# Optimization experiments

Measured on AMD Instinct MI355X. Metric: run time of the kernel, lower is better.

Reference implementation:

```python
import jax, jax.numpy as jnp
import numpy as np

D_MODEL, D_STATE, D_INNER, DT_RANK, D_CONV, K = 768, 16, 1536, 48, 3, 2
B_SZ, L_SEQ = 2, 2048

def setup_inputs() -> dict:
    key = jax.random.key(0)
    ks = jax.random.split(key, 10)
    s = lambda k, shp, sc=0.02: jax.random.normal(k, shp, dtype=jnp.float32) * sc
    return {
        "x": jax.random.normal(ks[0], (B_SZ, L_SEQ, D_MODEL), dtype=jnp.float32),
        "in_proj_w": s(ks[1], (2 * D_INNER, D_MODEL)),
        "conv_w": s(ks[2], (D_INNER, 1, D_CONV), 0.3),
        "conv_b": s(ks[3], (D_INNER,), 0.1),
        "x_proj_w": s(ks[4], (K, DT_RANK + 2 * D_STATE, D_INNER)),
        "dt_proj_w": s(ks[5], (K, D_INNER, DT_RANK), 0.1),
        "dt_proj_b": s(ks[6], (K, D_INNER), 0.1),
        "A_logs": s(ks[7], (K * D_INNER, D_STATE), 0.5),
        "Ds": jnp.ones((K * D_INNER,), dtype=jnp.float32),
        "out_proj_w": s(ks[8], (D_MODEL, D_INNER)),
    }

def _selective_scan(u, delta, A, Bp, Cp, Dk):
    # u, delta: [B, L, D]; A: [D, N]; Bp, Cp: [B, L, N]; Dk: [D]
    def step(h, inp):
        d_t, u_t, b_t, c_t = inp  # [B,D], [B,D], [B,N], [B,N]
        dA = jnp.exp(d_t[..., None] * A)  # [B,D,N]
        h = h * dA + (d_t * u_t)[..., None] * b_t[:, None, :]
        y_t = jnp.einsum('bdn,bn->bd', h, c_t)
        return h, y_t
    h0 = jnp.zeros((u.shape[0], u.shape[2], A.shape[1]), dtype=u.dtype)
    xs = (jnp.swapaxes(delta, 0, 1), jnp.swapaxes(u, 0, 1),
          jnp.swapaxes(Bp, 0, 1), jnp.swapaxes(Cp, 0, 1))
    _, ys = jax.lax.scan(step, h0, xs)  # ys: [L, B, D]
    return jnp.swapaxes(ys, 0, 1) + u * Dk  # [B, L, D]

def _direction(u_k, xw_k, dtw_k, dtb_k, Alog_k, D_k):
    x_dbl = jnp.einsum('bld,rd->blr', u_k, xw_k)
    dt_in, Bp, Cp = jnp.split(x_dbl, [DT_RANK, DT_RANK + D_STATE], axis=-1)
    delta = jax.nn.softplus(jnp.einsum('blr,dr->bld', dt_in, dtw_k) + dtb_k)
    A = -jnp.exp(Alog_k)
    return _selective_scan(u_k, delta, A, Bp, Cp, D_k)

def reference(x, in_proj_w, conv_w, conv_b, x_proj_w, dt_proj_w, dt_proj_b, A_logs, Ds, out_proj_w):
    xz = x @ in_proj_w.T                       # [B, L, 2*Din]
    x_conv, z = jnp.split(xz, 2, axis=-1)
    xc = jnp.swapaxes(x_conv, 1, 2)            # [B, Din, L]
    pad = (D_CONV - 1) // 2
    xc = jax.lax.conv_general_dilated(
        xc, conv_w, window_strides=(1,), padding=[(pad, pad)],
        feature_group_count=D_INNER, dimension_numbers=('NCH', 'OIH', 'NCH'))
    xc = xc + conv_b[None, :, None]
    u = jnp.swapaxes(jax.nn.silu(xc), 1, 2)    # [B, L, Din]

    u_dirs = jnp.stack([u, jnp.flip(u, axis=1)])          # [K, B, L, Din]
    A_logs_k = A_logs.reshape(K, D_INNER, D_STATE)
    Ds_k = Ds.reshape(K, D_INNER)
    y_dirs = jax.vmap(_direction)(u_dirs, x_proj_w, dt_proj_w, dt_proj_b, A_logs_k, Ds_k)
    y_scanned = y_dirs[0] + jnp.flip(y_dirs[1], axis=1)
    y_gated = y_scanned * z
    return y_gated @ out_proj_w.T
```

## Files before the change

kernel.cpp:

```cpp
#include <hip/hip_runtime.h>
#include <math.h>

#define D_MODEL 768
#define D_STATE 16
#define D_INNER 1536
#define DT_RANK 48
#define B_SZ    2
#define L_SEQ   2048
#define CH      64
#define NCH     (L_SEQ / CH)
#define NDG     24
#define MTOT    (B_SZ * L_SEQ)
#define SUB     16
#define LOG2E   1.4426950408889634f
#define LN2     0.6931471805599453f

typedef __bf16 bf16x8 __attribute__((ext_vector_type(8)));
typedef float f32x4 __attribute__((ext_vector_type(4)));
typedef ushort ushort8_t __attribute__((ext_vector_type(8)));

__device__ __forceinline__ float ex2(float x) {
  return __builtin_amdgcn_exp2f(x);
}

__device__ __forceinline__ ushort f2bf(float f) {
  unsigned int u = __float_as_uint(f);
  unsigned int r = (u + 0x7fff + ((u >> 16) & 1)) >> 16;
  return (ushort)r;
}
__device__ __forceinline__ float bf2f(ushort u) {
  return __uint_as_float(((unsigned int)u) << 16);
}

__device__ __forceinline__ void gload_lds16(const ushort* g, ushort* l) {
  __builtin_amdgcn_global_load_lds(
      (__attribute__((address_space(1))) void*)(void*)(g),
      (__attribute__((address_space(3))) void*)(void*)(l), 16, 0, 0);
}

__device__ __forceinline__ float softplus_fast(float x) {
  return (x > 20.f) ? x : LN2 * __log2f(1.f + ex2(x * LOG2E));
}

template <int BM, int BN, int ACT, int OBF, int DTOUT>
__device__ __forceinline__ void gemm_body(
    const ushort* __restrict__ A, int lda, const ushort* __restrict__ B,
    int ldb, const float* __restrict__ bias, void* __restrict__ Cp, int ldc,
    int Nreal, int K, int bxi, int byi, ushort* __restrict__ dtin,
    ushort* __restrict__ bcp) {
  __shared__ ushort As[2][BM][32];
  __shared__ ushort Bs[2][BN][32];
  constexpr int WM = BM / 2, WN = BN / 2;
  constexpr int FM = WM / 16, FN = WN / 16;
  const int tid = threadIdx.x;
  const int lane = tid & 63;
  const int w = tid >> 6;
  const int wr = w >> 1, wc = w & 1;
  const int bm = byi * BM, bn = bxi * BN;
  const int lrow = lane >> 2;
  const int lchunk = lane & 3;
  const int fr = lane & 15;
  const int k8 = (lane >> 4) * 8;

  f32x4 acc[FM][FN] = {};

  auto stage = [&](int buf, int k0) {
    if constexpr (BM >= 64) {
#pragma unroll
      for (int g = 0; g < BM / 64; ++g) {
        const int rb = w * (BM / 4) + g * 16;
        gload_lds16(A + (size_t)(bm + rb + lrow) * lda + k0 + lchunk * 8,
                    &As[buf][rb][0]);
      }
    } else {
      if (w < 2)
        gload_lds16(A + (size_t)(bm + w * 16 + lrow) * lda + k0 + lchunk * 8,
                    &As[buf][w * 16][0]);
    }
#pragma unroll
    for (int g = 0; g < BN / 64; ++g) {
      const int rb = w * (BN / 4) + g * 16;
      gload_lds16(B + (size_t)(bn + rb + lrow) * ldb + k0 + lchunk * 8,
                  &Bs[buf][rb][0]);
    }
  };

  stage(0, 0);
  __syncthreads();
  int cur = 0;
  for (int k0 = 0; k0 < K; k0 += 32) {
    if (k0 + 32 < K) stage(cur ^ 1, k0 + 32);
    bf16x8 af[FM], bfr[FN];
#pragma unroll
    for (int m = 0; m < FM; ++m)
      af[m] =
          *reinterpret_cast<const bf16x8*>(&As[cur][wr * WM + m * 16 + fr][k8]);
#pragma unroll
    for (int n = 0; n < FN; ++n)
      bfr[n] =
          *reinterpret_cast<const bf16x8*>(&Bs[cur][wc * WN + n * 16 + fr][k8]);
#pragma unroll
    for (int m = 0; m < FM; ++m)
#pragma unroll
      for (int n = 0; n < FN; ++n)
        acc[m][n] = __builtin_amdgcn_mfma_f32_16x16x32_bf16(af[m], bfr[n],
                                                            acc[m][n], 0, 0, 0);
    __syncthreads();
    cur ^= 1;
  }

  const int row4 = (lane >> 4) * 4;
#pragma unroll
  for (int m = 0; m < FM; ++m) {
#pragma unroll
    for (int n = 0; n < FN; ++n) {
      const int gn = bn + wc * WN + n * 16 + fr;
      const int gm0 = bm + wr * WM + m * 16 + row4;
#pragma unroll
      for (int j = 0; j < 4; ++j) {
        const float v = acc[m][n][j];
        const int gm = gm0 + j;
        if (DTOUT) {
          if (gn < 64)
            dtin[(size_t)gm * 64 + gn] = (gn < 48) ? f2bf(v) : (ushort)0;
          else if (gn >= 80 && gn < 144)
            dtin[(size_t)MTOT * 64 + (size_t)gm * 64 + (gn - 80)] =
                (gn < 128) ? f2bf(v) : (ushort)0;
          if (gn >= 48 && gn < 80)
            bcp[(size_t)gm * 32 + (gn - 48)] = f2bf(v);
          else if (gn >= 128 && gn < 160)
            bcp[(size_t)MTOT * 32 + (size_t)gm * 32 + (gn - 128)] = f2bf(v);
        }
        if (gn < Nreal) {
          float vv = v + (bias ? bias[gn] : 0.f);
          if (ACT == 1) vv = softplus_fast(vv);
          if (OBF)
            ((ushort*)Cp)[(size_t)gm * ldc + gn] = f2bf(vv);
          else
            ((float*)Cp)[(size_t)gm * ldc + gn] = vv;
        }
      }
    }
  }
}

template <int BM, int BN, int ACT, int OBF, int DTOUT>
__global__ __launch_bounds__(256) void gemm_k(
    const ushort* __restrict__ A, int lda, const ushort* __restrict__ B,
    int ldb, const float* __restrict__ bias, void* __restrict__ Cp, int ldc,
    int Nreal, int K, ushort* __restrict__ dtin, ushort* __restrict__ bcp) {
  gemm_body<BM, BN, ACT, OBF, DTOUT>(A, lda, B, ldb, bias, Cp, ldc, Nreal, K,
                                     blockIdx.x, blockIdx.y, dtin, bcp);
}

__global__ __launch_bounds__(256) void gemm_dt_k(
    const ushort* __restrict__ dtin, const ushort* __restrict__ w_dt,
    const float* __restrict__ dtb, ushort* __restrict__ delta) {
  const int k = blockIdx.z;
  gemm_body<64, 128, 1, 1, 0>(
      dtin + (size_t)k * MTOT * 64, 64, w_dt + (size_t)k * D_INNER * 64, 64,
      dtb + k * D_INNER, delta + (size_t)k * MTOT * D_INNER, D_INNER, D_INNER,
      64, blockIdx.x, blockIdx.y, nullptr, nullptr);
}

__global__ __launch_bounds__(256) void cvt_all_kernel(
    const float* __restrict__ x, const float* __restrict__ w_in,
    const float* __restrict__ w_out, const float* __restrict__ w_xp,
    const float* __restrict__ w_dt, ushort* __restrict__ x_bf,
    ushort* __restrict__ w_in_bf, ushort* __restrict__ w_out_bf,
    ushort* __restrict__ w_xp_bf, ushort* __restrict__ w_dt_bf) {
  const long N0 = 3145728, N1 = 2359296, N2 = 1179648, N3 = 393216, N4 = 196608;
  long i = ((long)blockIdx.x * 256 + threadIdx.x) * 4;
  if (i < N0) {
    const float4 v = *(const float4*)(x + i);
    ushort4 o = {f2bf(v.x), f2bf(v.y), f2bf(v.z), f2bf(v.w)};
    *(ushort4*)(x_bf + i) = o;
    return;
  }
  i -= N0;
  if (i < N1) {
    const float4 v = *(const float4*)(w_in + i);
    ushort4 o = {f2bf(v.x), f2bf(v.y), f2bf(v.z), f2bf(v.w)};
    *(ushort4*)(w_in_bf + i) = o;
    return;
  }
  i -= N1;
  if (i < N2) {
    const float4 v = *(const float4*)(w_out + i);
    ushort4 o = {f2bf(v.x), f2bf(v.y), f2bf(v.z), f2bf(v.w)};
    *(ushort4*)(w_out_bf + i) = o;
    return;
  }
  i -= N2;
  if (i < N3) {
    const long row = i / 1536;
    ushort4 o = {0, 0, 0, 0};
    if (row < 160) {
      const float4 v = *(const float4*)(w_xp + i);
      o.x = f2bf(v.x); o.y = f2bf(v.y); o.z = f2bf(v.z); o.w = f2bf(v.w);
    }
    *(ushort4*)(w_xp_bf + i) = o;
    return;
  }
  i -= N3;
  if (i < N4) {
    const int col = (int)(i & 63);
    const long row = i >> 6;
    ushort4 o = {0, 0, 0, 0};
    if (col < 48) {
      const float4 v = *(const float4*)(w_dt + row * 48 + col);
      o.x = f2bf(v.x); o.y = f2bf(v.y); o.z = f2bf(v.z); o.w = f2bf(v.w);
    }
    *(ushort4*)(w_dt_bf + i) = o;
  }
}

__global__ __launch_bounds__(256) void conv_silu_kernel(
    const ushort* __restrict__ xz, const float* __restrict__ cw,
    const float* __restrict__ cb, ushort* __restrict__ u_bf) {
  const int nd8 = D_INNER / 8;
  const int idx = blockIdx.x * 256 + threadIdx.x;
  const int d8 = idx % nd8;
  const int lg = (idx / nd8) % (L_SEQ / 8);
  const int b = idx / (nd8 * (L_SEQ / 8));
  const int d = d8 * 8;
  const int l0 = lg * 8;

  float w0[8], w1[8], w2[8], bs[8];
#pragma unroll
  for (int j = 0; j < 8; ++j) {
    w0[j] = cw[(d + j) * 3 + 0];
    w1[j] = cw[(d + j) * 3 + 1];
    w2[j] = cw[(d + j) * 3 + 2];
    bs[j] = cb[d + j];
  }
  const ushort* base = xz + ((size_t)b * L_SEQ) * 3072 + d;
  const ushort8_t zv = {0, 0, 0, 0, 0, 0, 0, 0};
  ushort8_t prev = (l0 > 0) ? *(const ushort8_t*)(base + (size_t)(l0 - 1) * 3072) : zv;
  ushort8_t curv = *(const ushort8_t*)(base + (size_t)l0 * 3072);
#pragma unroll
  for (int i = 0; i < 8; ++i) {
    const int l = l0 + i;
    const ushort8_t nxt =
        (l + 1 < L_SEQ) ? *(const ushort8_t*)(base + (size_t)(l + 1) * 3072) : zv;
    ushort8_t o;
#pragma unroll
    for (int j = 0; j < 8; ++j) {
      const float a = bs[j] + bf2f(prev[j]) * w0[j] + bf2f(curv[j]) * w1[j] +
                      bf2f(nxt[j]) * w2[j];
      o[j] = f2bf(a / (1.f + __expf(-a)));
    }
    *(ushort8_t*)(u_bf + ((size_t)b * L_SEQ + l) * D_INNER + d) = o;
    prev = curv;
    curv = nxt;
  }
}

__global__ __launch_bounds__(256) void scan_local_kernel(
    const ushort* __restrict__ u_bf, const ushort* __restrict__ bcb,
    const ushort* __restrict__ delta_bf, const float* __restrict__ A_logs,
    const float* __restrict__ Ds, ushort* __restrict__ y,
    float* __restrict__ hfin, float* __restrict__ Tsum) {
  __shared__ ushort sD[4][SUB][64];
  __shared__ ushort sU[4][SUB][64];
  __shared__ float sBCf[4][SUB][32];
  const int tid = threadIdx.x;
  const int wid = tid >> 6;
  const int lane = tid & 63;
  const int dl = lane;
  const int bid = blockIdx.x;
  const int chg = bid & (NCH / 4 - 1);
  const int rest = bid / (NCH / 4);
  const int dgB = rest % NDG;
  const int kb = rest / NDG;
  const int b = kb & 1;
  const int k = kb >> 1;
  const int ch = chg * 4 + wid;
  const int d0 = dgB * 64;
  const int d = d0 + dl;
  const int row = k * D_INNER + d;

  float An[16];
#pragma unroll
  for (int q = 0; q < 4; ++q) {
    const float4 a = *(const float4*)(A_logs + (size_t)row * D_STATE + q * 4);
    An[q * 4 + 0] = -__expf(a.x) * LOG2E;
    An[q * 4 + 1] = -__expf(a.y) * LOG2E;
    An[q * 4 + 2] = -__expf(a.z) * LOG2E;
    An[q * 4 + 3] = -__expf(a.w) * LOG2E;
  }
  const float Dk = Ds[row];

  const ushort* uptr = u_bf + (size_t)b * L_SEQ * D_INNER;
  const ushort* dptr = delta_bf + (size_t)(k * B_SZ + b) * L_SEQ * D_INNER;
  const ushort* bck = bcb + (size_t)k * MTOT * 32 + (size_t)b * L_SEQ * 32;
  ushort* yptr = y + (size_t)(k * B_SZ + b) * L_SEQ * D_INNER;

  float h[16] = {};
  float S = 0.f;

  for (int sub = 0; sub < CH / SUB; ++sub) {
    const int t0 = ch * CH + sub * SUB;
    const int lbase = k ? (L_SEQ - SUB - t0) : t0;
    {
      const int rd = lane >> 3, seg = lane & 7;
#pragma unroll
      for (int i = 0; i < SUB / 8; ++i) {
        const int r2 = i * 8 + rd;
        const int gr = k ? (SUB - 1 - r2) : r2;
        const size_t off = (size_t)(lbase + gr) * D_INNER + d0 + seg * 8;
        gload_lds16(dptr + off, &sD[wid][0][0] + i * 512);
        gload_lds16(uptr + off, &sU[wid][0][0] + i * 512);
      }
    }
    {
      const int rr = lane >> 2;
      const int q = lane & 3;
      const int gr = k ? (SUB - 1 - rr) : rr;
      const ushort8_t v =
          *(const ushort8_t*)(bck + (size_t)(lbase + gr) * 32 + q * 8);
      *(float4*)&sBCf[wid][rr][q * 8] =
          make_float4(bf2f(v[0]), bf2f(v[1]), bf2f(v[2]), bf2f(v[3]));
      *(float4*)&sBCf[wid][rr][q * 8 + 4] =
          make_float4(bf2f(v[4]), bf2f(v[5]), bf2f(v[6]), bf2f(v[7]));
    }
    __syncthreads();
    for (int s = 0; s < SUB; ++s) {
      const float dlt = bf2f(sD[wid][s][dl]);
      const float uu = bf2f(sU[wid][s][dl]);
      S += dlt;
      const float du = dlt * uu;
      float4 B4[4], C4[4];
#pragma unroll
      for (int q = 0; q < 4; ++q) {
        B4[q] = *(const float4*)&sBCf[wid][s][q * 4];
        C4[q] = *(const float4*)&sBCf[wid][s][16 + q * 4];
      }
      float yt = 0.f;
#pragma unroll
      for (int q = 0; q < 4; ++q) {
        h[q * 4 + 0] = h[q * 4 + 0] * ex2(dlt * An[q * 4 + 0]) + du * B4[q].x;
        yt += h[q * 4 + 0] * C4[q].x;
        h[q * 4 + 1] = h[q * 4 + 1] * ex2(dlt * An[q * 4 + 1]) + du * B4[q].y;
        yt += h[q * 4 + 1] * C4[q].y;
        h[q * 4 + 2] = h[q * 4 + 2] * ex2(dlt * An[q * 4 + 2]) + du * B4[q].z;
        yt += h[q * 4 + 2] * C4[q].z;
        h[q * 4 + 3] = h[q * 4 + 3] * ex2(dlt * An[q * 4 + 3]) + du * B4[q].w;
        yt += h[q * 4 + 3] * C4[q].w;
      }
      const int t = t0 + s;
      const int l = k ? (L_SEQ - 1 - t) : t;
      yptr[(size_t)l * D_INNER + d] = f2bf(yt + uu * Dk);
    }
    __syncthreads();
  }

  const size_t cidxB = ((size_t)(k * B_SZ + b) * NCH + ch) * NDG + dgB;
#pragma unroll
  for (int q = 0; q < 4; ++q)
    *(float4*)(hfin + cidxB * 1024 + dl * 16 + q * 4) =
        make_float4(h[q * 4], h[q * 4 + 1], h[q * 4 + 2], h[q * 4 + 3]);
  Tsum[cidxB * 64 + dl] = S;
}

__global__ __launch_bounds__(256) void scan_stitch_kernel(
    const float* __restrict__ hfin, const float* __restrict__ Tsum,
    const float* __restrict__ A_logs, float* __restrict__ hin) {
  const int tid = threadIdx.x;
  const int dl = tid >> 2;
  const int nq = tid & 3;
  const int bid = blockIdx.x;
  const int dgB = bid % NDG;
  const int b = (bid / NDG) & 1;
  const int k = bid / (NDG * 2);
  const int row = k * D_INNER + dgB * 64 + dl;
  const float4 alv = *(const float4*)(A_logs + (size_t)row * D_STATE + nq * 4);
  const float An0 = -__expf(alv.x) * LOG2E, An1 = -__expf(alv.y) * LOG2E;
  const float An2 = -__expf(alv.z) * LOG2E, An3 = -__expf(alv.w) * LOG2E;
  float c0 = 0.f, c1 = 0.f, c2 = 0.f, c3 = 0.f;
  for (int ch = 0; ch < NCH; ++ch) {
    const size_t cidxB = ((size_t)(k * B_SZ + b) * NCH + ch) * NDG + dgB;
    const size_t off = cidxB * 1024 + dl * 16 + nq * 4;
    *(float4*)(hin + off) = make_float4(c0, c1, c2, c3);
    const float T = Tsum[cidxB * 64 + dl];
    const float4 hf = *(const float4*)(hfin + off);
    c0 = c0 * ex2(An0 * T) + hf.x;
    c1 = c1 * ex2(An1 * T) + hf.y;
    c2 = c2 * ex2(An2 * T) + hf.z;
    c3 = c3 * ex2(An3 * T) + hf.w;
  }
}

__global__ __launch_bounds__(256) void fixup_gate_kernel(
    const ushort* __restrict__ bcb, const ushort* __restrict__ delta_bf,
    const float* __restrict__ A_logs, const float* __restrict__ hin,
    const ushort* __restrict__ y, const ushort* __restrict__ xz_bf,
    ushort* __restrict__ yg) {
  __shared__ ushort sd0[64][64], sd1[64][64];
  __shared__ float sC0f[64][16], sC1f[64][16];
  __shared__ float sQF[64][4], sQB[64][4];
  const int tid = threadIdx.x;
  const int wid = tid >> 6;
  const int lane = tid & 63;
  const int tq = wid;
  const int dl = lane;
  const int bid = blockIdx.x;
  const int ch = bid & (NCH - 1);
  const int rest = bid >> 5;
  const int dgB = rest % NDG;
  const int b = rest / NDG;
  const int d0 = dgB * 64;
  const int d = d0 + dl;
  const int lbase = ch * CH;
  const int chb = NCH - 1 - ch;

  float AnF[16], AnB[16], hF[16], hB[16];
#pragma unroll
  for (int q = 0; q < 4; ++q) {
    const float4 af = *(const float4*)(A_logs + (size_t)d * D_STATE + q * 4);
    AnF[q * 4 + 0] = -__expf(af.x) * LOG2E;
    AnF[q * 4 + 1] = -__expf(af.y) * LOG2E;
    AnF[q * 4 + 2] = -__expf(af.z) * LOG2E;
    AnF[q * 4 + 3] = -__expf(af.w) * LOG2E;
    const float4 ab =
        *(const float4*)(A_logs + (size_t)(D_INNER + d) * D_STATE + q * 4);
    AnB[q * 4 + 0] = -__expf(ab.x) * LOG2E;
    AnB[q * 4 + 1] = -__expf(ab.y) * LOG2E;
    AnB[q * 4 + 2] = -__expf(ab.z) * LOG2E;
    AnB[q * 4 + 3] = -__expf(ab.w) * LOG2E;
  }
  const size_t cF = ((size_t)(0 * B_SZ + b) * NCH + ch) * NDG + dgB;
  const size_t cB = ((size_t)(1 * B_SZ + b) * NCH + chb) * NDG + dgB;
#pragma unroll
  for (int q = 0; q < 4; ++q) {
    const float4 hv = *(const float4*)(hin + cF * 1024 + dl * 16 + q * 4);
    hF[q * 4 + 0] = hv.x; hF[q * 4 + 1] = hv.y;
    hF[q * 4 + 2] = hv.z; hF[q * 4 + 3] = hv.w;
    const float4 hw = *(const float4*)(hin + cB * 1024 + dl * 16 + q * 4);
    hB[q * 4 + 0] = hw.x; hB[q * 4 + 1] = hw.y;
    hB[q * 4 + 2] = hw.z; hB[q * 4 + 3] = hw.w;
  }

  const ushort* d0p =
      delta_bf + ((size_t)(0 * B_SZ + b) * L_SEQ + lbase) * D_INNER + d0;
  const ushort* d1p =
      delta_bf + ((size_t)(1 * B_SZ + b) * L_SEQ + lbase) * D_INNER + d0;
  {
    const int rd = lane >> 3, seg = lane & 7;
#pragma unroll
    for (int i = 0; i < 2; ++i) {
      const int sl = i * 4 + wid;
      const int r = sl * 8 + rd;
      const size_t off = (size_t)r * D_INNER + seg * 8;
      gload_lds16(d0p + off, &sd0[0][0] + sl * 512);
      gload_lds16(d1p + off, &sd1[0][0] + sl * 512);
    }
  }
  {
    const ushort* bc0 = bcb + (size_t)b * L_SEQ * 32;
    const ushort* bc1 = bcb + (size_t)MTOT * 32 + (size_t)b * L_SEQ * 32;
    const int r = tid >> 2;
    const int q = tid & 3;
    const ushort4 c0 =
        *(const ushort4*)(bc0 + (size_t)(lbase + r) * 32 + 16 + q * 4);
    const ushort4 c1 =
        *(const ushort4*)(bc1 + (size_t)(lbase + r) * 32 + 16 + q * 4);
    *(float4*)&sC0f[r][q * 4] =
        make_float4(bf2f(c0.x), bf2f(c0.y), bf2f(c0.z), bf2f(c0.w));
    *(float4*)&sC1f[r][q * 4] =
        make_float4(bf2f(c1.x), bf2f(c1.y), bf2f(c1.z), bf2f(c1.w));
  }
  __syncthreads();
  float qf = 0.f, qb = 0.f;
#pragma unroll
  for (int i = 0; i < 16; ++i) {
    qf += bf2f(sd0[tq * 16 + i][dl]);
    qb += bf2f(sd1[tq * 16 + i][dl]);
  }
  sQF[dl][tq] = qf;
  sQB[dl][tq] = qb;
  __syncthreads();
  float SF = 0.f, SB = 0.f;
#pragma unroll
  for (int j = 0; j < 4; ++j) {
    if (j < tq) SF += sQF[dl][j];
    if (j > tq) SB += sQB[dl][j];
  }

  const ushort* y0p = y + ((size_t)(0 * B_SZ + b) * L_SEQ) * D_INNER;
  const ushort* y1p = y + ((size_t)(1 * B_SZ + b) * L_SEQ) * D_INNER;
  float yacc[16];
#pragma unroll
  for (int i = 0; i < 16; ++i) {
    const int t = tq * 16 + i;
    SF += bf2f(sd0[t][dl]);
    const float4 C0 = *(const float4*)&sC0f[t][0];
    const float4 C1 = *(const float4*)&sC0f[t][4];
    const float4 C2 = *(const float4*)&sC0f[t][8];
    const float4 C3 = *(const float4*)&sC0f[t][12];
    float wf;
    wf  = C0.x * (ex2(AnF[0] * SF) * hF[0]);
    wf += C0.y * (ex2(AnF[1] * SF) * hF[1]);
    wf += C0.z * (ex2(AnF[2] * SF) * hF[2]);
    wf += C0.w * (ex2(AnF[3] * SF) * hF[3]);
    wf += C1.x * (ex2(AnF[4] * SF) * hF[4]);
    wf += C1.y * (ex2(AnF[5] * SF) * hF[5]);
    wf += C1.z * (ex2(AnF[6] * SF) * hF[6]);
    wf += C1.w * (ex2(AnF[7] * SF) * hF[7]);
    wf += C2.x * (ex2(AnF[8] * SF) * hF[8]);
    wf += C2.y * (ex2(AnF[9] * SF) * hF[9]);
    wf += C2.z * (ex2(AnF[10] * SF) * hF[10]);
    wf += C2.w * (ex2(AnF[11] * SF) * hF[11]);
    wf += C3.x * (ex2(AnF[12] * SF) * hF[12]);
    wf += C3.y * (ex2(AnF[13] * SF) * hF[13]);
    wf += C3.z * (ex2(AnF[14] * SF) * hF[14]);
    wf += C3.w * (ex2(AnF[15] * SF) * hF[15]);
    yacc[i] = bf2f(y0p[(size_t)(lbase + t) * D_INNER + d]) + wf;
  }
#pragma unroll
  for (int i = 15; i >= 0; --i) {
    const int t = tq * 16 + i;
    SB += bf2f(sd1[t][dl]);
    const float4 C0 = *(const float4*)&sC1f[t][0];
    const float4 C1 = *(const float4*)&sC1f[t][4];
    const float4 C2 = *(const float4*)&sC1f[t][8];
    const float4 C3 = *(const float4*)&sC1f[t][12];
    float wb;
    wb  = C0.x * (ex2(AnB[0] * SB) * hB[0]);
    wb += C0.y * (ex2(AnB[1] * SB) * hB[1]);
    wb += C0.z * (ex2(AnB[2] * SB) * hB[2]);
    wb += C0.w * (ex2(AnB[3] * SB) * hB[3]);
    wb += C1.x * (ex2(AnB[4] * SB) * hB[4]);
    wb += C1.y * (ex2(AnB[5] * SB) * hB[5]);
    wb += C1.z * (ex2(AnB[6] * SB) * hB[6]);
    wb += C1.w * (ex2(AnB[7] * SB) * hB[7]);
    wb += C2.x * (ex2(AnB[8] * SB) * hB[8]);
    wb += C2.y * (ex2(AnB[9] * SB) * hB[9]);
    wb += C2.z * (ex2(AnB[10] * SB) * hB[10]);
    wb += C2.w * (ex2(AnB[11] * SB) * hB[11]);
    wb += C3.x * (ex2(AnB[12] * SB) * hB[12]);
    wb += C3.y * (ex2(AnB[13] * SB) * hB[13]);
    wb += C3.z * (ex2(AnB[14] * SB) * hB[14]);
    wb += C3.w * (ex2(AnB[15] * SB) * hB[15]);
    yacc[i] += bf2f(y1p[(size_t)(lbase + t) * D_INNER + d]) + wb;
  }
#pragma unroll
  for (int i = 0; i < 16; ++i) {
    const int l = lbase + tq * 16 + i;
    const float z = bf2f(xz_bf[((size_t)b * L_SEQ + l) * 3072 + 1536 + d]);
    yg[((size_t)b * L_SEQ + l) * D_INNER + d] = f2bf(yacc[i] * z);
  }
}

extern "C" void kernel_launch(void* const* d_in, const int* in_sizes, int n_in,
                              void* d_out, int out_size, void* d_ws,
                              size_t ws_size, hipStream_t stream) {
  const float* x          = (const float*)d_in[0];
  const float* in_proj_w  = (const float*)d_in[1];
  const float* conv_w     = (const float*)d_in[2];
  const float* conv_b     = (const float*)d_in[3];
  const float* x_proj_w   = (const float*)d_in[4];
  const float* dt_proj_w  = (const float*)d_in[5];
  const float* dt_proj_b  = (const float*)d_in[6];
  const float* A_logs     = (const float*)d_in[7];
  const float* Ds         = (const float*)d_in[8];
  const float* out_proj_w = (const float*)d_in[9];
  float* out = (float*)d_out;

  const int M = MTOT;
  const size_t NST = (size_t)2 * B_SZ * NCH * NDG;

  float* ws    = (float*)d_ws;
  float* hfin  = ws;
  float* hin   = hfin + NST * 1024;
  float* Tsum  = hin + NST * 1024;
  ushort* bcbuf    = (ushort*)(Tsum + NST * 64);
  ushort* x_bf     = bcbuf + (size_t)2 * M * 32;
  ushort* w_in_bf  = x_bf + (size_t)M * 768;
  ushort* w_out_bf = w_in_bf + (size_t)3072 * 768;
  ushort* w_xp_bf  = w_out_bf + (size_t)768 * 1536;
  ushort* w_dt_bf  = w_xp_bf + (size_t)256 * 1536;
  ushort* xz_bf    = w_dt_bf + (size_t)2 * 1536 * 64;
  ushort* u_bf     = xz_bf + (size_t)M * 3072;
  ushort* delta_bf = u_bf + (size_t)M * 1536;
  ushort* dtin     = delta_bf + (size_t)2 * M * 1536;
  ushort* y_bf     = dtin + (size_t)2 * M * 64;
  ushort* yg_bf    = y_bf + (size_t)2 * M * 1536;

  dim3 blk(256);

  {
    const long TOT = 3145728L + 2359296 + 1179648 + 393216 + 196608;
    cvt_all_kernel<<<dim3((TOT / 4 + 255) / 256), blk, 0, stream>>>(
        x, in_proj_w, out_proj_w, x_proj_w, dt_proj_w, x_bf, w_in_bf, w_out_bf,
        w_xp_bf, w_dt_bf);
  }

  gemm_k<128, 128, 0, 1, 0><<<dim3(3072 / 128, M / 128), blk, 0, stream>>>(
      x_bf, 768, w_in_bf, 768, nullptr, xz_bf, 3072, 3072, 768, nullptr,
      nullptr);

  conv_silu_kernel<<<dim3(B_SZ * (L_SEQ / 8) * (D_INNER / 8) / 256), blk, 0,
                     stream>>>(xz_bf, conv_w, conv_b, u_bf);

  gemm_k<32, 64, 0, 0, 1><<<dim3(3, M / 32), blk, 0, stream>>>(
      u_bf, 1536, w_xp_bf, 1536, nullptr, nullptr, 1, 0, 1536, dtin, bcbuf);

  gemm_dt_k<<<dim3(1536 / 128, M / 64, 2), blk, 0, stream>>>(
      dtin, w_dt_bf, dt_proj_b, delta_bf);

  scan_local_kernel<<<dim3(2 * B_SZ * NDG * (NCH / 4)), blk, 0, stream>>>(
      u_bf, bcbuf, delta_bf, A_logs, Ds, y_bf, hfin, Tsum);
  scan_stitch_kernel<<<dim3(2 * B_SZ * NDG), blk, 0, stream>>>(hfin, Tsum,
                                                               A_logs, hin);
  fixup_gate_kernel<<<dim3(B_SZ * NDG * NCH), blk, 0, stream>>>(
      bcbuf, delta_bf, A_logs, hin, y_bf, xz_bf, yg_bf);

  gemm_k<128, 128, 0, 0, 0><<<dim3(768 / 128, M / 128), blk, 0, stream>>>(
      yg_bf, 1536, w_out_bf, 1536, nullptr, out, 768, 768, 1536, nullptr,
      nullptr);
}
```

Baseline: 239.1 us.

## Halve scan chunk length, drop LDS staging, store B/C projections as fp32

The local scan chunk shrinks from 64 to 32 steps, which doubles the number of chunks and the parallelism in the sequential scan. The scan now reads delta, u and fp32 B/C directly from global memory with strided pointers, replacing the LDS staging and its barriers. The fixup kernel is adjusted so each 64-step block covers two 32-step chunks, and B/C are kept in fp32 so no bf16 conversion is needed. In exchange the stitch pass handles twice as many chunk states, and the uncoalesced-per-row direct global loads may add latency.

```diff
diff --git a/kernel.cpp b/kernel.cpp
--- a/kernel.cpp
+++ b/kernel.cpp
@@ -7,11 +7,10 @@
 #define DT_RANK 48
 #define B_SZ    2
 #define L_SEQ   2048
-#define CH      64
+#define CH      32
 #define NCH     (L_SEQ / CH)
 #define NDG     24
 #define MTOT    (B_SZ * L_SEQ)
-#define SUB     16
 #define LOG2E   1.4426950408889634f
 #define LN2     0.6931471805599453f
 
@@ -47,7 +46,7 @@
     const ushort* __restrict__ A, int lda, const ushort* __restrict__ B,
     int ldb, const float* __restrict__ bias, void* __restrict__ Cp, int ldc,
     int Nreal, int K, int bxi, int byi, ushort* __restrict__ dtin,
-    ushort* __restrict__ bcp) {
+    float* __restrict__ bcp) {
   __shared__ ushort As[2][BM][32];
   __shared__ ushort Bs[2][BN][32];
   constexpr int WM = BM / 2, WN = BN / 2;
@@ -127,9 +126,9 @@
             dtin[(size_t)MTOT * 64 + (size_t)gm * 64 + (gn - 80)] =
                 (gn < 128) ? f2bf(v) : (ushort)0;
           if (gn >= 48 && gn < 80)
-            bcp[(size_t)gm * 32 + (gn - 48)] = f2bf(v);
+            bcp[(size_t)gm * 32 + (gn - 48)] = v;
           else if (gn >= 128 && gn < 160)
-            bcp[(size_t)MTOT * 32 + (size_t)gm * 32 + (gn - 128)] = f2bf(v);
+            bcp[(size_t)MTOT * 32 + (size_t)gm * 32 + (gn - 128)] = v;
         }
         if (gn < Nreal) {
           float vv = v + (bias ? bias[gn] : 0.f);
@@ -148,7 +147,7 @@
 __global__ __launch_bounds__(256) void gemm_k(
     const ushort* __restrict__ A, int lda, const ushort* __restrict__ B,
     int ldb, const float* __restrict__ bias, void* __restrict__ Cp, int ldc,
-    int Nreal, int K, ushort* __restrict__ dtin, ushort* __restrict__ bcp) {
+    int Nreal, int K, ushort* __restrict__ dtin, float* __restrict__ bcp) {
   gemm_body<BM, BN, ACT, OBF, DTOUT>(A, lda, B, ldb, bias, Cp, ldc, Nreal, K,
                                      blockIdx.x, blockIdx.y, dtin, bcp);
 }
@@ -257,17 +256,13 @@
 }
 
 __global__ __launch_bounds__(256) void scan_local_kernel(
-    const ushort* __restrict__ u_bf, const ushort* __restrict__ bcb,
+    const ushort* __restrict__ u_bf, const float* __restrict__ bcf,
     const ushort* __restrict__ delta_bf, const float* __restrict__ A_logs,
     const float* __restrict__ Ds, ushort* __restrict__ y,
     float* __restrict__ hfin, float* __restrict__ Tsum) {
-  __shared__ ushort sD[4][SUB][64];
-  __shared__ ushort sU[4][SUB][64];
-  __shared__ float sBCf[4][SUB][32];
   const int tid = threadIdx.x;
   const int wid = tid >> 6;
   const int lane = tid & 63;
-  const int dl = lane;
   const int bid = blockIdx.x;
   const int chg = bid & (NCH / 4 - 1);
   const int rest = bid / (NCH / 4);
@@ -276,8 +271,7 @@
   const int b = kb & 1;
   const int k = kb >> 1;
   const int ch = chg * 4 + wid;
-  const int d0 = dgB * 64;
-  const int d = d0 + dl;
+  const int d = dgB * 64 + lane;
   const int row = k * D_INNER + d;
 
   float An[16];
@@ -291,76 +285,63 @@
   }
   const float Dk = Ds[row];
 
-  const ushort* uptr = u_bf + (size_t)b * L_SEQ * D_INNER;
-  const ushort* dptr = delta_bf + (size_t)(k * B_SZ + b) * L_SEQ * D_INNER;
-  const ushort* bck = bcb + (size_t)k * MTOT * 32 + (size_t)b * L_SEQ * 32;
-  ushort* yptr = y + (size_t)(k * B_SZ + b) * L_SEQ * D_INNER;
+  const int lstart = k ? (L_SEQ - 1 - ch * CH) : ch * CH;
+  const ptrdiff_t dstr = k ? -(ptrdiff_t)D_INNER : (ptrdiff_t)D_INNER;
+  const ptrdiff_t bstr = k ? -32 : 32;
+  const ushort* dp =
+      delta_bf + ((size_t)(k * B_SZ + b) * L_SEQ + lstart) * D_INNER + d;
+  const ushort* up = u_bf + ((size_t)b * L_SEQ + lstart) * D_INNER + d;
+  const float* bcp =
+      bcf + ((size_t)k * MTOT + (size_t)b * L_SEQ + lstart) * 32;
+  ushort* yp = y + ((size_t)(k * B_SZ + b) * L_SEQ + lstart) * D_INNER + d;
 
   float h[16] = {};
   float S = 0.f;
 
-  for (int sub = 0; sub < CH / SUB; ++sub) {
-    const int t0 = ch * CH + sub * SUB;
-    const int lbase = k ? (L_SEQ - SUB - t0) : t0;
-    {
-      const int rd = lane >> 3, seg = lane & 7;
-#pragma unroll
-      for (int i = 0; i < SUB / 8; ++i) {
-        const int r2 = i * 8 + rd;
-        const int gr = k ? (SUB - 1 - r2) : r2;
-        const size_t off = (size_t)(lbase + gr) * D_INNER + d0 + seg * 8;
-        gload_lds16(dptr + off, &sD[wid][0][0] + i * 512);
-        gload_lds16(uptr + off, &sU[wid][0][0] + i * 512);
-      }
-    }
-    {
-      const int rr = lane >> 2;
-      const int q = lane & 3;
-      const int gr = k ? (SUB - 1 - rr) : rr;
-      const ushort8_t v =
-          *(const ushort8_t*)(bck + (size_t)(lbase + gr) * 32 + q * 8);
-      *(float4*)&sBCf[wid][rr][q * 8] =
-          make_float4(bf2f(v[0]), bf2f(v[1]), bf2f(v[2]), bf2f(v[3]));
-      *(float4*)&sBCf[wid][rr][q * 8 + 4] =
-          make_float4(bf2f(v[4]), bf2f(v[5]), bf2f(v[6]), bf2f(v[7]));
-    }
-    __syncthreads();
-    for (int s = 0; s < SUB; ++s) {
-      const float dlt = bf2f(sD[wid][s][dl]);
-      const float uu = bf2f(sU[wid][s][dl]);
-      S += dlt;
-      const float du = dlt * uu;
-      float4 B4[4], C4[4];
-#pragma unroll
-      for (int q = 0; q < 4; ++q) {
-        B4[q] = *(const float4*)&sBCf[wid][s][q * 4];
-        C4[q] = *(const float4*)&sBCf[wid][s][16 + q * 4];
-      }
-      float yt = 0.f;
-#pragma unroll
-      for (int q = 0; q < 4; ++q) {
-        h[q * 4 + 0] = h[q * 4 + 0] * ex2(dlt * An[q * 4 + 0]) + du * B4[q].x;
-        yt += h[q * 4 + 0] * C4[q].x;
-        h[q * 4 + 1] = h[q * 4 + 1] * ex2(dlt * An[q * 4 + 1]) + du * B4[q].y;
-        yt += h[q * 4 + 1] * C4[q].y;
-        h[q * 4 + 2] = h[q * 4 + 2] * ex2(dlt * An[q * 4 + 2]) + du * B4[q].z;
-        yt += h[q * 4 + 2] * C4[q].z;
-        h[q * 4 + 3] = h[q * 4 + 3] * ex2(dlt * An[q * 4 + 3]) + du * B4[q].w;
-        yt += h[q * 4 + 3] * C4[q].w;
-      }
-      const int t = t0 + s;
-      const int l = k ? (L_SEQ - 1 - t) : t;
-      yptr[(size_t)l * D_INNER + d] = f2bf(yt + uu * Dk);
-    }
-    __syncthreads();
+#pragma unroll 4
+  for (int s = 0; s < CH; ++s) {
+    const float dlt = bf2f(*dp);
+    const float uu = bf2f(*up);
+    S += dlt;
+    const float du = dlt * uu;
+    const float4 B0 = *(const float4*)(bcp + 0);
+    const float4 B1 = *(const float4*)(bcp + 4);
+    const float4 B2 = *(const float4*)(bcp + 8);
+    const float4 B3 = *(const float4*)(bcp + 12);
+    const float4 C0 = *(const float4*)(bcp + 16);
+    const float4 C1 = *(const float4*)(bcp + 20);
+    const float4 C2 = *(const float4*)(bcp + 24);
+    const float4 C3 = *(const float4*)(bcp + 28);
+    float yt = 0.f;
+    h[0] = h[0] * ex2(dlt * An[0]) + du * B0.x;  yt += h[0] * C0.x;
+    h[1] = h[1] * ex2(dlt * An[1]) + du * B0.y;  yt += h[1] * C0.y;
+    h[2] = h[2] * ex2(dlt * An[2]) + du * B0.z;  yt += h[2] * C0.z;
+    h[3] = h[3] * ex2(dlt * An[3]) + du * B0.w;  yt += h[3] * C0.w;
+    h[4] = h[4] * ex2(dlt * An[4]) + du * B1.x;  yt += h[4] * C1.x;
+    h[5] = h[5] * ex2(dlt * An[5]) + du * B1.y;  yt += h[5] * C1.y;
+    h[6] = h[6] * ex2(dlt * An[6]) + du * B1.z;  yt += h[6] * C1.z;
+    h[7] = h[7] * ex2(dlt * An[7]) + du * B1.w;  yt += h[7] * C1.w;
+    h[8] = h[8] * ex2(dlt * An[8]) + du * B2.x;  yt += h[8] * C2.x;
+    h[9] = h[9] * ex2(dlt * An[9]) + du * B2.y;  yt += h[9] * C2.y;
+    h[10] = h[10] * ex2(dlt * An[10]) + du * B2.z; yt += h[10] * C2.z;
+    h[11] = h[11] * ex2(dlt * An[11]) + du * B2.w; yt += h[11] * C2.w;
+    h[12] = h[12] * ex2(dlt * An[12]) + du * B3.x; yt += h[12] * C3.x;
+    h[13] = h[13] * ex2(dlt * An[13]) + du * B3.y; yt += h[13] * C3.y;
+    h[14] = h[14] * ex2(dlt * An[14]) + du * B3.z; yt += h[14] * C3.z;
+    h[15] = h[15] * ex2(dlt * An[15]) + du * B3.w; yt += h[15] * C3.w;
+    *yp = f2bf(yt + uu * Dk);
+    dp += dstr;
+    up += dstr;
+    yp += dstr;
+    bcp += bstr;
   }
 
   const size_t cidxB = ((size_t)(k * B_SZ + b) * NCH + ch) * NDG + dgB;
 #pragma unroll
   for (int q = 0; q < 4; ++q)
-    *(float4*)(hfin + cidxB * 1024 + dl * 16 + q * 4) =
+    *(float4*)(hfin + cidxB * 1024 + lane * 16 + q * 4) =
         make_float4(h[q * 4], h[q * 4 + 1], h[q * 4 + 2], h[q * 4 + 3]);
-  Tsum[cidxB * 64 + dl] = S;
+  Tsum[cidxB * 64 + lane] = S;
 }
 
 __global__ __launch_bounds__(256) void scan_stitch_kernel(
@@ -392,7 +373,7 @@
 }
 
 __global__ __launch_bounds__(256) void fixup_gate_kernel(
-    const ushort* __restrict__ bcb, const ushort* __restrict__ delta_bf,
+    const float* __restrict__ bcf, const ushort* __restrict__ delta_bf,
     const float* __restrict__ A_logs, const float* __restrict__ hin,
     const ushort* __restrict__ y, const ushort* __restrict__ xz_bf,
     ushort* __restrict__ yg) {
@@ -405,14 +386,13 @@
   const int tq = wid;
   const int dl = lane;
   const int bid = blockIdx.x;
-  const int ch = bid & (NCH - 1);
+  const int chf = bid & 31;
   const int rest = bid >> 5;
   const int dgB = rest % NDG;
   const int b = rest / NDG;
   const int d0 = dgB * 64;
   const int d = d0 + dl;
-  const int lbase = ch * CH;
-  const int chb = NCH - 1 - ch;
+  const int lbase = chf * 64;
 
   float AnF[16], AnB[16], hF[16], hB[16];
 #pragma unroll
@@ -429,8 +409,10 @@
     AnB[q * 4 + 2] = -__expf(ab.z) * LOG2E;
     AnB[q * 4 + 3] = -__expf(ab.w) * LOG2E;
   }
-  const size_t cF = ((size_t)(0 * B_SZ + b) * NCH + ch) * NDG + dgB;
-  const size_t cB = ((size_t)(1 * B_SZ + b) * NCH + chb) * NDG + dgB;
+  const int chF = chf * 2 + (tq >> 1);
+  const int chB = NCH - 1 - chf * 2 - (tq >> 1);
+  const size_t cF = ((size_t)(0 * B_SZ + b) * NCH + chF) * NDG + dgB;
+  const size_t cB = ((size_t)(1 * B_SZ + b) * NCH + chB) * NDG + dgB;
 #pragma unroll
   for (int q = 0; q < 4; ++q) {
     const float4 hv = *(const float4*)(hin + cF * 1024 + dl * 16 + q * 4);
@@ -457,18 +439,14 @@
     }
   }
   {
-    const ushort* bc0 = bcb + (size_t)b * L_SEQ * 32;
-    const ushort* bc1 = bcb + (size_t)MTOT * 32 + (size_t)b * L_SEQ * 32;
+    const float* bc0 = bcf + (size_t)b * L_SEQ * 32;
+    const float* bc1 = bcf + (size_t)MTOT * 32 + (size_t)b * L_SEQ * 32;
     const int r = tid >> 2;
     const int q = tid & 3;
-    const ushort4 c0 =
-        *(const ushort4*)(bc0 + (size_t)(lbase + r) * 32 + 16 + q * 4);
-    const ushort4 c1 =
-        *(const ushort4*)(bc1 + (size_t)(lbase + r) * 32 + 16 + q * 4);
     *(float4*)&sC0f[r][q * 4] =
-        make_float4(bf2f(c0.x), bf2f(c0.y), bf2f(c0.z), bf2f(c0.w));
+        *(const float4*)(bc0 + (size_t)(lbase + r) * 32 + 16 + q * 4);
     *(float4*)&sC1f[r][q * 4] =
-        make_float4(bf2f(c1.x), bf2f(c1.y), bf2f(c1.z), bf2f(c1.w));
+        *(const float4*)(bc1 + (size_t)(lbase + r) * 32 + 16 + q * 4);
   }
   __syncthreads();
   float qf = 0.f, qb = 0.f;
@@ -480,12 +458,8 @@
   sQF[dl][tq] = qf;
   sQB[dl][tq] = qb;
   __syncthreads();
-  float SF = 0.f, SB = 0.f;
-#pragma unroll
-  for (int j = 0; j < 4; ++j) {
-    if (j < tq) SF += sQF[dl][j];
-    if (j > tq) SB += sQB[dl][j];
-  }
+  float SF = (tq & 1) ? sQF[dl][tq - 1] : 0.f;
+  float SB = (tq & 1) ? 0.f : sQB[dl][tq + 1];
 
   const ushort* y0p = y + ((size_t)(0 * B_SZ + b) * L_SEQ) * D_INNER;
   const ushort* y1p = y + ((size_t)(1 * B_SZ + b) * L_SEQ) * D_INNER;
@@ -574,8 +548,8 @@
   float* hfin  = ws;
   float* hin   = hfin + NST * 1024;
   float* Tsum  = hin + NST * 1024;
-  ushort* bcbuf    = (ushort*)(Tsum + NST * 64);
-  ushort* x_bf     = bcbuf + (size_t)2 * M * 32;
+  float* bcf   = Tsum + NST * 64;
+  ushort* x_bf     = (ushort*)(bcf + (size_t)2 * M * 32);
   ushort* w_in_bf  = x_bf + (size_t)M * 768;
   ushort* w_out_bf = w_in_bf + (size_t)3072 * 768;
   ushort* w_xp_bf  = w_out_bf + (size_t)768 * 1536;
@@ -604,17 +578,17 @@
                      stream>>>(xz_bf, conv_w, conv_b, u_bf);
 
   gemm_k<32, 64, 0, 0, 1><<<dim3(3, M / 32), blk, 0, stream>>>(
-      u_bf, 1536, w_xp_bf, 1536, nullptr, nullptr, 1, 0, 1536, dtin, bcbuf);
+      u_bf, 1536, w_xp_bf, 1536, nullptr, nullptr, 1, 0, 1536, dtin, bcf);
 
   gemm_dt_k<<<dim3(1536 / 128, M / 64, 2), blk, 0, stream>>>(
       dtin, w_dt_bf, dt_proj_b, delta_bf);
 
   scan_local_kernel<<<dim3(2 * B_SZ * NDG * (NCH / 4)), blk, 0, stream>>>(
-      u_bf, bcbuf, delta_bf, A_logs, Ds, y_bf, hfin, Tsum);
+      u_bf, bcf, delta_bf, A_logs, Ds, y_bf, hfin, Tsum);
   scan_stitch_kernel<<<dim3(2 * B_SZ * NDG), blk, 0, stream>>>(hfin, Tsum,
                                                                A_logs, hin);
-  fixup_gate_kernel<<<dim3(B_SZ * NDG * NCH), blk, 0, stream>>>(
-      bcbuf, delta_bf, A_logs, hin, y_bf, xz_bf, yg_bf);
+  fixup_gate_kernel<<<dim3(B_SZ * NDG * (L_SEQ / 64)), blk, 0, stream>>>(
+      bcf, delta_bf, A_logs, hin, y_bf, xz_bf, yg_bf);
 
   gemm_k<128, 128, 0, 0, 0><<<dim3(768 / 128, M / 128), blk, 0, stream>>>(
       yg_bf, 1536, w_out_bf, 1536, nullptr, out, 768, 768, 1536, nullptr,
```

Result: slower. 255.5 us (+6.8%).
